# Kernel optimization log

Measured on AMD Instinct MI355X. Metric: run time of the kernel, lower is better.

Reference implementation:

```python
import jax, jax.numpy as jnp
import numpy as np

BATCH, C_IN, C_OUT, H, K = 32, 128, 256, 56, 3

def setup_inputs() -> dict:
    key = jax.random.key(0)
    k1, k2 = jax.random.split(key)
    img = jax.random.normal(k1, (BATCH, C_IN, H, H), dtype=jnp.float32)
    # matches nn.Parameter((rand - 0.5) * (1 / (C_IN * K**2)))
    filtro = (jax.random.uniform(k2, (C_OUT, C_IN, K, K), dtype=jnp.float32) - 0.5) * (1.0 / (C_IN * K * K))
    return {"img": img, "filtro": filtro}

def reference(img, filtro):
    # Original: padding=0 (stride=1), im2col unfold + matmul == VALID cross-correlation.
    return jax.lax.conv_general_dilated(
        img, filtro,
        window_strides=(1, 1),
        padding="VALID",
        dimension_numbers=("NCHW", "OIHW", "NCHW"),
    )  # -> [BATCH, C_OUT, H-K+1, H-K+1]
```

## Files before the change

kernel.cpp:

```cpp
#include <hip/hip_runtime.h>


#define BB   32
#define CIN  128
#define COUT 256
#define HH   56
#define WW   56
#define OH   54
#define OW   54

typedef short bf16x8 __attribute__((ext_vector_type(8)));
typedef float f32x4  __attribute__((ext_vector_type(4)));
typedef unsigned short u16x8 __attribute__((ext_vector_type(8)));

#define GLOAD_LDS16(g, l) __builtin_amdgcn_global_load_lds( \
    (const __attribute__((address_space(1))) unsigned int*)(g), \
    (__attribute__((address_space(3))) unsigned int*)(l), 16, 0, 0)

static __device__ __forceinline__ unsigned short f2bf(float f) {
    unsigned int u = __float_as_uint(f);
    u += 0x7FFFu + ((u >> 16) & 1u);
    return (unsigned short)(u >> 16);
}

__global__ __launch_bounds__(256) void prep_img(const float* __restrict__ img,
                                                unsigned short* __restrict__ imgT) {
    const int b = blockIdx.x / HH;
    const int y = blockIdx.x - b * HH;
    for (int i = threadIdx.x; i < 16 * WW; i += 256) {
        const int g = i / WW;
        const int x = i - g * WW;
        unsigned short pk[8];
        #pragma unroll
        for (int j = 0; j < 8; ++j)
            pk[j] = f2bf(img[((size_t)(b * CIN + g * 8 + j) * HH + y) * WW + x]);
        *(u16x8*)(imgT + ((size_t)(b * HH + y) * WW + x) * CIN + g * 8) = *(u16x8*)pk;
    }
}

__global__ __launch_bounds__(256) void prep_flt(const float* __restrict__ flt,
                                                unsigned short* __restrict__ filtF) {
    const int idx = blockIdx.x * 256 + threadIdx.x;
    const int co = idx >> 7;
    const int ci = idx & 127;
    const int cot = co >> 6, col = co & 63;
    const int m = col >> 4, sub = col & 15;
    const int c = ci >> 5, kg = (ci >> 3) & 3, e = ci & 7;
    const size_t base = (size_t)cot * 73728 + sub * 512 + m * 128 + c * 32 + kg * 8 + e;
    #pragma unroll
    for (int t = 0; t < 9; ++t)
        filtF[base + t * 8192] = f2bf(flt[(size_t)(co * CIN + ci) * 9 + t]);
}

#define IMG_ROWB   896
#define IMG_PLANE  9216
#define IMG_BUF    36864
#define FA_OFF     73728
#define FB_OFF     98304
#define LDS_BYTES  110592

static __device__ __forceinline__ int dpp_ror8(int x) {
    return __builtin_amdgcn_update_dpp(0, x, 0x128, 0xF, 0xF, true);
}
static __device__ __forceinline__ bf16x8 rot8(bf16x8 v) {
    union { bf16x8 h; int i[4]; } u, r;
    u.h = v;
    #pragma unroll
    for (int k = 0; k < 4; ++k) r.i[k] = dpp_ror8(u.i[k]);
    return r.h;
}
static __device__ __forceinline__ bf16x8 sel8(bool c0, bf16x8 a, bf16x8 b) {
    union { bf16x8 h; int i[4]; } ua, ub, o;
    ua.h = a; ub.h = b;
    #pragma unroll
    for (int k = 0; k < 4; ++k) o.i[k] = c0 ? ua.i[k] : ub.i[k];
    return o.h;
}

template<int DX, int S0>
static __device__ __forceinline__ void do_dx(const char* __restrict__ aBase,
                                             const char* __restrict__ bBc,
                                             const bool ysub0,
                                             f32x4 (&acc)[2][7])
{
    bf16x8 b0[7], b2[7];
    #pragma unroll
    for (int nf = 0; nf < 7; ++nf)
        b0[nf] = *(const bf16x8*)(bBc + (nf * 8 + DX) * 16);
    #pragma unroll
    for (int nf = 0; nf < 7; ++nf)
        b2[nf] = *(const bf16x8*)(bBc + 2 * IMG_ROWB + (nf * 8 + DX) * 16);

    {
        bf16x8 a0 = *(const bf16x8*)(aBase + (S0 + 0) * 4096);
        bf16x8 a1 = *(const bf16x8*)(aBase + (S0 + 0) * 4096 + 256);
        #pragma unroll
        for (int nf = 0; nf < 7; ++nf) {
            acc[0][nf] = __builtin_amdgcn_mfma_f32_16x16x32_bf16(a0, b0[nf], acc[0][nf], 0, 0, 0);
            acc[1][nf] = __builtin_amdgcn_mfma_f32_16x16x32_bf16(a1, b0[nf], acc[1][nf], 0, 0, 0);
        }
    }
    {
        bf16x8 a0 = *(const bf16x8*)(aBase + (S0 + 1) * 4096);
        bf16x8 a1 = *(const bf16x8*)(aBase + (S0 + 1) * 4096 + 256);
        #pragma unroll
        for (int nf = 0; nf < 7; ++nf) {
            bf16x8 b1 = sel8(ysub0, rot8(b0[nf]), rot8(b2[nf]));
            acc[0][nf] = __builtin_amdgcn_mfma_f32_16x16x32_bf16(a0, b1, acc[0][nf], 0, 0, 0);
            acc[1][nf] = __builtin_amdgcn_mfma_f32_16x16x32_bf16(a1, b1, acc[1][nf], 0, 0, 0);
        }
    }
    {
        bf16x8 a0 = *(const bf16x8*)(aBase + (S0 + 2) * 4096);
        bf16x8 a1 = *(const bf16x8*)(aBase + (S0 + 2) * 4096 + 256);
        #pragma unroll
        for (int nf = 0; nf < 7; ++nf) {
            acc[0][nf] = __builtin_amdgcn_mfma_f32_16x16x32_bf16(a0, b2[nf], acc[0][nf], 0, 0, 0);
            acc[1][nf] = __builtin_amdgcn_mfma_f32_16x16x32_bf16(a1, b2[nf], acc[1][nf], 0, 0, 0);
        }
    }
}

static __device__ __forceinline__ constexpr int tapA(int s) {
    return (s < 3) ? 3 * s : 3 * (s - 3) + 1;
}

template<int C>
static __device__ __forceinline__ void conv_iter(
    const unsigned short* __restrict__ imgT,
    const unsigned short* __restrict__ fcot,
    const int flane, const int hi, const int tid,
    char* __restrict__ pFA, char* __restrict__ pFB,
    char* __restrict__ sdstI,
    const char* __restrict__ bB, const char* __restrict__ aA, const char* __restrict__ aB,
    const int (&gsite)[5], const bool ysub0,
    f32x4 (&acc)[2][7])
{
    {
        GLOAD_LDS16(fcot + flane + (hi ? 5 : 2) * 8192 + C * 32, pFB + tid * 16);
        if (tid < 256)
            GLOAD_LDS16(fcot + flane + 8 * 8192 + C * 32, pFB + 8192 + tid * 16);
    }
    if constexpr (C < 3) {
        char* d = sdstI + ((C + 1) & 1) * IMG_BUF;
        #pragma unroll
        for (int k = 0; k < 5; ++k)
            if (gsite[k] >= 0)
                GLOAD_LDS16(imgT + gsite[k] + (C + 1) * 32, d + k * 1024);
    }
    const char* bBc = bB + (C & 1) * IMG_BUF;
    do_dx<0, 0>(aA, bBc, ysub0, acc);
    do_dx<1, 3>(aA, bBc, ysub0, acc);
    __syncthreads();
    if constexpr (C < 3) {
        GLOAD_LDS16(fcot + flane + (hi ? tapA(1) : tapA(0)) * 8192 + (C + 1) * 32, pFA + 0 * 8192 + tid * 16);
        GLOAD_LDS16(fcot + flane + (hi ? tapA(3) : tapA(2)) * 8192 + (C + 1) * 32, pFA + 1 * 8192 + tid * 16);
        GLOAD_LDS16(fcot + flane + (hi ? tapA(5) : tapA(4)) * 8192 + (C + 1) * 32, pFA + 2 * 8192 + tid * 16);
    }
    do_dx<2, 0>(aB, bBc, ysub0, acc);
    __syncthreads();
}

__global__ __launch_bounds__(512, 1) void conv_mfma(
    const unsigned short* __restrict__ imgT,
    const unsigned short* __restrict__ filtF,
    float* __restrict__ out)
{
    __shared__ char lds[LDS_BYTES];

    const int tid  = threadIdx.x;
    const int lane = tid & 63, w8 = tid >> 6;
    const int rp   = w8 >> 1, mh = w8 & 1;
    const int sub  = lane & 15, kg = lane >> 4;
    const int ysub = sub >> 3,  xl = sub & 7;
    const bool ysub0 = (ysub == 0);
    const int hi = tid >> 8;

    const int w    = (blockIdx.x & 7) * 112 + (blockIdx.x >> 3);
    const int cot  = w & 3;
    const int rest = w >> 2;
    const int strip = rest % 7;
    const int b     = rest / 7;
    const int co0   = cot * 64;
    const int ystart = (strip < 6) ? strip * 8 : (OH - 8);

    char* const pImg = lds;
    char* const pFA  = lds + FA_OFF;
    char* const pFB  = lds + FB_OFF;
    const char* bB = pImg + kg * IMG_PLANE + (2 * rp + ysub) * IMG_ROWB + xl * 16;
    const char* aA = pFA + kg * 1024 + mh * 512 + sub * 16;
    const char* aB = pFB + kg * 1024 + mh * 512 + sub * 16;

    const unsigned short* fcot = filtF + (size_t)cot * 73728;
    const int flane = ((tid & 15) * 512) + (((tid >> 4) & 3) * 128) + (((tid >> 6) & 3) * 8);

    char* sdstI = pImg + rp * IMG_PLANE + (mh * 320 + lane) * 16;
    int gsite[5];
    #pragma unroll
    for (int k = 0; k < 5; ++k) {
        const int site = mh * 320 + k * 64 + lane;
        const int rr = site / 56;
        const int xx = site - rr * 56;
        gsite[k] = (site < 560)
                 ? ((b * HH + ystart + rr) * WW + xx) * CIN + rp * 8
                 : -1;
    }

    f32x4 acc[2][7];
    #pragma unroll
    for (int mm = 0; mm < 2; ++mm)
        #pragma unroll
        for (int nf = 0; nf < 7; ++nf) acc[mm][nf] = (f32x4)0.0f;

    #pragma unroll
    for (int k = 0; k < 5; ++k)
        if (gsite[k] >= 0)
            GLOAD_LDS16(imgT + gsite[k], sdstI + k * 1024);
    GLOAD_LDS16(fcot + flane + (hi ? tapA(1) : tapA(0)) * 8192, pFA + 0 * 8192 + tid * 16);
    GLOAD_LDS16(fcot + flane + (hi ? tapA(3) : tapA(2)) * 8192, pFA + 1 * 8192 + tid * 16);
    GLOAD_LDS16(fcot + flane + (hi ? tapA(5) : tapA(4)) * 8192, pFA + 2 * 8192 + tid * 16);
    __syncthreads();

    conv_iter<0>(imgT, fcot, flane, hi, tid, pFA, pFB, sdstI, bB, aA, aB, gsite, ysub0, acc);
    conv_iter<1>(imgT, fcot, flane, hi, tid, pFA, pFB, sdstI, bB, aA, aB, gsite, ysub0, acc);
    conv_iter<2>(imgT, fcot, flane, hi, tid, pFA, pFB, sdstI, bB, aA, aB, gsite, ysub0, acc);
    conv_iter<3>(imgT, fcot, flane, hi, tid, pFA, pFB, sdstI, bB, aA, aB, gsite, ysub0, acc);

    const int y = ystart + 2 * rp + ysub;
    #pragma unroll
    for (int mm = 0; mm < 2; ++mm) {
        const int cob = co0 + (mh * 2 + mm) * 16 + kg * 4;
        #pragma unroll
        for (int nf = 0; nf < 7; ++nf) {
            const int x = nf * 8 + xl;
            if (x < OW) {
                float* o = out + ((size_t)(b * COUT + cob) * OH + y) * OW + x;
                #pragma unroll
                for (int j = 0; j < 4; ++j)
                    o[(size_t)j * OH * OW] = acc[mm][nf][j];
            }
        }
    }
}

#define COB  16
#define THF  6
#define CIBF 2
#define IRF  (THF + 2)
__global__ __launch_bounds__(256) void conv3x3_fp32(
    const float* __restrict__ img, const float* __restrict__ flt,
    float* __restrict__ out)
{
    __shared__ float si[CIBF][IRF][WW];
    __shared__ float sf[CIBF][COB][9];
    const int tid = threadIdx.x;
    const int tx  = tid & 63;
    const int tg  = tid >> 6;
    int bid = blockIdx.x;
    const int ytile = bid % (OH / THF);  bid /= (OH / THF);
    const int cob   = bid % (COUT / COB); bid /= (COUT / COB);
    const int b     = bid;
    const int y0  = ytile * THF;
    const int co0 = cob * COB;
    float acc[4][THF];
    #pragma unroll
    for (int c = 0; c < 4; ++c)
        #pragma unroll
        for (int y = 0; y < THF; ++y) acc[c][y] = 0.0f;
    for (int ci0 = 0; ci0 < CIN; ci0 += CIBF) {
        for (int i = tid; i < CIBF * IRF * (WW / 4); i += 256) {
            const int cil = i / (IRF * (WW / 4));
            int rem = i - cil * (IRF * (WW / 4));
            const int r = rem / (WW / 4);
            const int v = rem - r * (WW / 4);
            const float4* src = reinterpret_cast<const float4*>(
                img + (((size_t)b * CIN + (ci0 + cil)) * HH + (y0 + r)) * WW) + v;
            reinterpret_cast<float4*>(&si[cil][r][0])[v] = *src;
        }
        for (int i = tid; i < CIBF * COB * 9; i += 256) {
            const int cil = i / (COB * 9);
            int rem = i - cil * (COB * 9);
            const int col = rem / 9;
            const int e   = rem - col * 9;
            sf[cil][col][e] = flt[(((size_t)(co0 + col)) * CIN + (ci0 + cil)) * 9 + e];
        }
        __syncthreads();
        if (tx < OW) {
            #pragma unroll
            for (int cil = 0; cil < CIBF; ++cil) {
                float f[4][9];
                #pragma unroll
                for (int c = 0; c < 4; ++c)
                    #pragma unroll
                    for (int e = 0; e < 9; ++e) f[c][e] = sf[cil][tg * 4 + c][e];
                float a[IRF][3];
                #pragma unroll
                for (int r = 0; r < IRF; ++r) {
                    a[r][0] = si[cil][r][tx + 0];
                    a[r][1] = si[cil][r][tx + 1];
                    a[r][2] = si[cil][r][tx + 2];
                }
                #pragma unroll
                for (int y = 0; y < THF; ++y)
                    #pragma unroll
                    for (int dy = 0; dy < 3; ++dy)
                        #pragma unroll
                        for (int c = 0; c < 4; ++c)
                            acc[c][y] = fmaf(a[y + dy][0], f[c][dy * 3 + 0],
                                        fmaf(a[y + dy][1], f[c][dy * 3 + 1],
                                        fmaf(a[y + dy][2], f[c][dy * 3 + 2], acc[c][y])));
            }
        }
        __syncthreads();
    }
    if (tx < OW) {
        #pragma unroll
        for (int c = 0; c < 4; ++c) {
            const int co = co0 + tg * 4 + c;
            #pragma unroll
            for (int y = 0; y < THF; ++y)
                out[(((size_t)b * COUT + co) * OH + (y0 + y)) * OW + tx] = acc[c][y];
        }
    }
}

extern "C" void kernel_launch(void* const* d_in, const int* in_sizes, int n_in,
                              void* d_out, int out_size, void* d_ws, size_t ws_size,
                              hipStream_t stream) {
    const float* img = (const float*)d_in[0];
    const float* flt = (const float*)d_in[1];
    float* out = (float*)d_out;

    const size_t IMGT_BYTES = (size_t)BB * HH * WW * CIN * 2;
    const size_t FILT_BYTES = (size_t)4 * 73728 * 2;
    if (ws_size < IMGT_BYTES + FILT_BYTES) {
        conv3x3_fp32<<<BB * (COUT / COB) * (OH / THF), 256, 0, stream>>>(img, flt, out);
        return;
    }
    unsigned short* imgT  = (unsigned short*)d_ws;
    unsigned short* filtF = (unsigned short*)((char*)d_ws + IMGT_BYTES);

    prep_img<<<BB * HH, 256, 0, stream>>>(img, imgT);
    prep_flt<<<(COUT * CIN) / 256, 256, 0, stream>>>(flt, filtF);
    conv_mfma<<<4 * 7 * BB, 512, 0, stream>>>(imgT, filtF, out);
}
```

Before: 114.2 us.

## Double-buffer filter alongside image and split loading by wave role

Filter taps now get a full double buffer in LDS next to the image buffers, which raises LDS use to 144KB. Each channel chunk therefore needs one barrier instead of two, and the filter no longer has to be reloaded piecewise between dx phases. Waves 0-3 stage image rows and waves 4-7 stage all nine filter taps, each through a uniform nine-load pattern with no per-site predicates. MFMA sections run under raised s_setprio, and an explicit vmcnt wait plus barrier replaces __syncthreads, which risks exposing load latency at each chunk boundary.

Measured after the change: 112.4 us. About the same (-1.6%).

```diff
diff --git a/kernel.cpp b/kernel.cpp
--- a/kernel.cpp
+++ b/kernel.cpp
@@ -54,10 +54,9 @@
 
 #define IMG_ROWB   896
 #define IMG_PLANE  9216
-#define IMG_BUF    36864
-#define FA_OFF     73728
-#define FB_OFF     98304
-#define LDS_BYTES  110592
+#define BUF_SZ     36864
+#define FLT_OFF    73728
+#define LDS_BYTES  147456
 
 static __device__ __forceinline__ int dpp_ror8(int x) {
     return __builtin_amdgcn_update_dpp(0, x, 0x128, 0xF, 0xF, true);
@@ -77,8 +76,8 @@
     return o.h;
 }
 
-template<int DX, int S0>
-static __device__ __forceinline__ void do_dx(const char* __restrict__ aBase,
+template<int DX>
+static __device__ __forceinline__ void do_dx(const char* __restrict__ aB,
                                              const char* __restrict__ bBc,
                                              const bool ysub0,
                                              f32x4 (&acc)[2][7])
@@ -92,8 +91,8 @@
         b2[nf] = *(const bf16x8*)(bBc + 2 * IMG_ROWB + (nf * 8 + DX) * 16);
 
     {
-        bf16x8 a0 = *(const bf16x8*)(aBase + (S0 + 0) * 4096);
-        bf16x8 a1 = *(const bf16x8*)(aBase + (S0 + 0) * 4096 + 256);
+        bf16x8 a0 = *(const bf16x8*)(aB + (DX + 0) * 4096);
+        bf16x8 a1 = *(const bf16x8*)(aB + (DX + 0) * 4096 + 256);
         #pragma unroll
         for (int nf = 0; nf < 7; ++nf) {
             acc[0][nf] = __builtin_amdgcn_mfma_f32_16x16x32_bf16(a0, b0[nf], acc[0][nf], 0, 0, 0);
@@ -101,8 +100,8 @@
         }
     }
     {
-        bf16x8 a0 = *(const bf16x8*)(aBase + (S0 + 1) * 4096);
-        bf16x8 a1 = *(const bf16x8*)(aBase + (S0 + 1) * 4096 + 256);
+        bf16x8 a0 = *(const bf16x8*)(aB + (DX + 3) * 4096);
+        bf16x8 a1 = *(const bf16x8*)(aB + (DX + 3) * 4096 + 256);
         #pragma unroll
         for (int nf = 0; nf < 7; ++nf) {
             bf16x8 b1 = sel8(ysub0, rot8(b0[nf]), rot8(b2[nf]));
@@ -111,8 +110,8 @@
         }
     }
     {
-        bf16x8 a0 = *(const bf16x8*)(aBase + (S0 + 2) * 4096);
-        bf16x8 a1 = *(const bf16x8*)(aBase + (S0 + 2) * 4096 + 256);
+        bf16x8 a0 = *(const bf16x8*)(aB + (DX + 6) * 4096);
+        bf16x8 a1 = *(const bf16x8*)(aB + (DX + 6) * 4096 + 256);
         #pragma unroll
         for (int nf = 0; nf < 7; ++nf) {
             acc[0][nf] = __builtin_amdgcn_mfma_f32_16x16x32_bf16(a0, b2[nf], acc[0][nf], 0, 0, 0);
@@ -121,44 +120,38 @@
     }
 }
 
-static __device__ __forceinline__ constexpr int tapA(int s) {
-    return (s < 3) ? 3 * s : 3 * (s - 3) + 1;
+template<int CN>
+static __device__ __forceinline__ void stage_all(
+    const unsigned short* __restrict__ gsrc,
+    char* __restrict__ dbase,
+    const int (&offs)[9])
+{
+    char* d = dbase + (CN & 1) * BUF_SZ;
+    #pragma unroll
+    for (int r = 0; r < 9; ++r)
+        GLOAD_LDS16(gsrc + offs[r] + CN * 32, d + r * 1024);
 }
 
 template<int C>
 static __device__ __forceinline__ void conv_iter(
-    const unsigned short* __restrict__ imgT,
-    const unsigned short* __restrict__ fcot,
-    const int flane, const int hi, const int tid,
-    char* __restrict__ pFA, char* __restrict__ pFB,
-    char* __restrict__ sdstI,
-    const char* __restrict__ bB, const char* __restrict__ aA, const char* __restrict__ aB,
-    const int (&gsite)[5], const bool ysub0,
-    f32x4 (&acc)[2][7])
-{
-    {
-        GLOAD_LDS16(fcot + flane + (hi ? 5 : 2) * 8192 + C * 32, pFB + tid * 16);
-        if (tid < 256)
-            GLOAD_LDS16(fcot + flane + 8 * 8192 + C * 32, pFB + 8192 + tid * 16);
-    }
+    const unsigned short* __restrict__ gsrc,
+    char* __restrict__ dbase, const int (&offs)[9],
+    const char* __restrict__ aBase, const char* __restrict__ bBbase,
+    const bool ysub0, f32x4 (&acc)[2][7])
+{
+    if constexpr (C < 3) stage_all<C + 1>(gsrc, dbase, offs);
+    const char* aB  = aBase  + (C & 1) * BUF_SZ;
+    const char* bBc = bBbase + (C & 1) * BUF_SZ;
+    __builtin_amdgcn_s_setprio(1);
+    do_dx<0>(aB, bBc, ysub0, acc);
+    do_dx<1>(aB, bBc, ysub0, acc);
+    do_dx<2>(aB, bBc, ysub0, acc);
+    __builtin_amdgcn_s_setprio(0);
     if constexpr (C < 3) {
-        char* d = sdstI + ((C + 1) & 1) * IMG_BUF;
-        #pragma unroll
-        for (int k = 0; k < 5; ++k)
-            if (gsite[k] >= 0)
-                GLOAD_LDS16(imgT + gsite[k] + (C + 1) * 32, d + k * 1024);
-    }
-    const char* bBc = bB + (C & 1) * IMG_BUF;
-    do_dx<0, 0>(aA, bBc, ysub0, acc);
-    do_dx<1, 3>(aA, bBc, ysub0, acc);
-    __syncthreads();
-    if constexpr (C < 3) {
-        GLOAD_LDS16(fcot + flane + (hi ? tapA(1) : tapA(0)) * 8192 + (C + 1) * 32, pFA + 0 * 8192 + tid * 16);
-        GLOAD_LDS16(fcot + flane + (hi ? tapA(3) : tapA(2)) * 8192 + (C + 1) * 32, pFA + 1 * 8192 + tid * 16);
-        GLOAD_LDS16(fcot + flane + (hi ? tapA(5) : tapA(4)) * 8192 + (C + 1) * 32, pFA + 2 * 8192 + tid * 16);
-    }
-    do_dx<2, 0>(aB, bBc, ysub0, acc);
-    __syncthreads();
+        asm volatile("s_waitcnt vmcnt(0)" ::: "memory");
+        __builtin_amdgcn_s_barrier();
+        __builtin_amdgcn_sched_barrier(0);
+    }
 }
 
 __global__ __launch_bounds__(512, 1) void conv_mfma(
@@ -174,7 +167,6 @@
     const int sub  = lane & 15, kg = lane >> 4;
     const int ysub = sub >> 3,  xl = sub & 7;
     const bool ysub0 = (ysub == 0);
-    const int hi = tid >> 8;
 
     const int w    = (blockIdx.x & 7) * 112 + (blockIdx.x >> 3);
     const int cot  = w & 3;
@@ -185,25 +177,35 @@
     const int ystart = (strip < 6) ? strip * 8 : (OH - 8);
 
     char* const pImg = lds;
-    char* const pFA  = lds + FA_OFF;
-    char* const pFB  = lds + FB_OFF;
-    const char* bB = pImg + kg * IMG_PLANE + (2 * rp + ysub) * IMG_ROWB + xl * 16;
-    const char* aA = pFA + kg * 1024 + mh * 512 + sub * 16;
-    const char* aB = pFB + kg * 1024 + mh * 512 + sub * 16;
-
+    char* const pFlt = lds + FLT_OFF;
+    const char* bBbase = pImg + kg * IMG_PLANE + (2 * rp + ysub) * IMG_ROWB + xl * 16;
+    const char* aBase  = pFlt + kg * 1024 + mh * 512 + sub * 16;
     const unsigned short* fcot = filtF + (size_t)cot * 73728;
-    const int flane = ((tid & 15) * 512) + (((tid >> 4) & 3) * 128) + (((tid >> 6) & 3) * 8);
-
-    char* sdstI = pImg + rp * IMG_PLANE + (mh * 320 + lane) * 16;
-    int gsite[5];
-    #pragma unroll
-    for (int k = 0; k < 5; ++k) {
-        const int site = mh * 320 + k * 64 + lane;
-        const int rr = site / 56;
-        const int xx = site - rr * 56;
-        gsite[k] = (site < 560)
-                 ? ((b * HH + ystart + rr) * WW + xx) * CIN + rp * 8
-                 : -1;
+
+    const unsigned short* gsrc;
+    char* dbase;
+    int offs[9];
+    if (w8 < 4) {
+        gsrc  = imgT;
+        dbase = pImg + w8 * IMG_PLANE + lane * 16;
+        #pragma unroll
+        for (int r = 0; r < 9; ++r) {
+            const int site = r * 64 + lane;
+            const int rr = site / 56;
+            const int xx = site - rr * 56;
+            const int off = ((b * HH + ystart + rr) * WW + xx) * CIN + w8 * 8;
+            offs[r] = (site < 560) ? off : offs[0];
+        }
+    } else {
+        const int v = w8 - 4;
+        gsrc  = fcot;
+        dbase = pFlt + v * 9216 + lane * 16;
+        const int flane = (lane & 15) * 512 + (lane >> 4) * 128;
+        #pragma unroll
+        for (int r = 0; r < 9; ++r) {
+            const int q = v * 9 + r;
+            offs[r] = (q >> 2) * 8192 + (q & 3) * 8 + flane;
+        }
     }
 
     f32x4 acc[2][7];
@@ -212,19 +214,15 @@
         #pragma unroll
         for (int nf = 0; nf < 7; ++nf) acc[mm][nf] = (f32x4)0.0f;
 
-    #pragma unroll
-    for (int k = 0; k < 5; ++k)
-        if (gsite[k] >= 0)
-            GLOAD_LDS16(imgT + gsite[k], sdstI + k * 1024);
-    GLOAD_LDS16(fcot + flane + (hi ? tapA(1) : tapA(0)) * 8192, pFA + 0 * 8192 + tid * 16);
-    GLOAD_LDS16(fcot + flane + (hi ? tapA(3) : tapA(2)) * 8192, pFA + 1 * 8192 + tid * 16);
-    GLOAD_LDS16(fcot + flane + (hi ? tapA(5) : tapA(4)) * 8192, pFA + 2 * 8192 + tid * 16);
-    __syncthreads();
-
-    conv_iter<0>(imgT, fcot, flane, hi, tid, pFA, pFB, sdstI, bB, aA, aB, gsite, ysub0, acc);
-    conv_iter<1>(imgT, fcot, flane, hi, tid, pFA, pFB, sdstI, bB, aA, aB, gsite, ysub0, acc);
-    conv_iter<2>(imgT, fcot, flane, hi, tid, pFA, pFB, sdstI, bB, aA, aB, gsite, ysub0, acc);
-    conv_iter<3>(imgT, fcot, flane, hi, tid, pFA, pFB, sdstI, bB, aA, aB, gsite, ysub0, acc);
+    stage_all<0>(gsrc, dbase, offs);
+    asm volatile("s_waitcnt vmcnt(0)" ::: "memory");
+    __builtin_amdgcn_s_barrier();
+    __builtin_amdgcn_sched_barrier(0);
+
+    conv_iter<0>(gsrc, dbase, offs, aBase, bBbase, ysub0, acc);
+    conv_iter<1>(gsrc, dbase, offs, aBase, bBbase, ysub0, acc);
+    conv_iter<2>(gsrc, dbase, offs, aBase, bBbase, ysub0, acc);
+    conv_iter<3>(gsrc, dbase, offs, aBase, bBbase, ysub0, acc);
 
     const int y = ystart + 2 * rp + ysub;
     #pragma unroll
```
